# Kernel optimization log

Measured on AMD Instinct MI355X. Metric: run time of the kernel, lower is better.

Reference implementation:

```python
import jax, jax.numpy as jnp
import numpy as np

SCALE = 8.0  # sqrt(head_dim=64); module divides scores by self.scale


def setup_inputs() -> dict:
    key = jax.random.key(0)
    kq, kk, kv = jax.random.split(key, 3)
    B, H, L, D = 4, 8, 2048, 64
    queries = jax.random.normal(kq, (B, H, L, D), dtype=jnp.float32)
    keys = jax.random.normal(kk, (B, H, L, D), dtype=jnp.float32)
    values = jax.random.normal(kv, (B, H, L, D), dtype=jnp.float32)
    return {"queries": queries, "keys": keys, "values": values}


def reference(queries, keys, values):
    # scores: [B, H, L_Q, L_K]
    L_Q, L_K = queries.shape[2], keys.shape[2]
    scores = jnp.einsum('bnqd,bnkd->bnqk', queries, keys) / SCALE
    # causal mask: triu(ones, diagonal=1) positions set to -inf
    causal = jnp.triu(jnp.ones((L_Q, L_K), dtype=bool), k=1)
    scores = jnp.where(causal[None, None, :, :], -jnp.inf, scores)
    A = jax.nn.softmax(scores, axis=-1)  # dropout p=0.0 (eval) -> identity
    V = jnp.einsum('bnqk,bnkd->bnqd', A, values)
    return V
```

## Files before the change

kernel.cpp:

```cpp
#include <hip/hip_runtime.h>
#include <hip/hip_bf16.h>

typedef __attribute__((ext_vector_type(8))) short bf16x8;
typedef __attribute__((ext_vector_type(16))) float f32x16;

#define DHEAD 64
#define L_SEQ 2048
#define QSCALE (0.125f * 1.44269504088896340736f)

union U4S8 { uint4 u; bf16x8 s; };

__device__ __forceinline__ unsigned pk2(float a, float b) {
    unsigned r;
    asm("v_cvt_pk_bf16_f32 %0, %1, %2" : "=v"(r) : "v"(a), "v"(b));
    return r;
}

__device__ __forceinline__ float fexp2(float x) {
#if __has_builtin(__builtin_amdgcn_exp2f)
    return __builtin_amdgcn_exp2f(x);
#else
    return __expf(x * 0.69314718055994530942f);
#endif
}

#define MAX16(P) fmaxf(fmaxf(fmaxf(fmaxf(P[0],P[1]),fmaxf(P[2],P[3])),          \
                             fmaxf(fmaxf(P[4],P[5]),fmaxf(P[6],P[7]))),         \
                       fmaxf(fmaxf(fmaxf(P[8],P[9]),fmaxf(P[10],P[11])),        \
                             fmaxf(fmaxf(P[12],P[13]),fmaxf(P[14],P[15]))))
#define SUM16(P) ((((P[0]+P[1])+(P[2]+P[3]))+((P[4]+P[5])+(P[6]+P[7])))         \
                + (((P[8]+P[9])+(P[10]+P[11]))+((P[12]+P[13])+(P[14]+P[15]))))


__global__ __launch_bounds__(256, 2)
void fattn_kernel(const float* __restrict__ Qg, const float* __restrict__ Kg,
                  const float* __restrict__ Vg, float* __restrict__ Og) {
    __shared__ uint4 sK4[2][16][64];
    __shared__ uint4 sV4[2][16][64];

    const int tid  = threadIdx.x;
    const int lane = tid & 63;
    const int w    = tid >> 6;
    const int hi   = lane >> 5;
    const int c    = lane & 31;

    const int id  = blockIdx.x;
    const int bh  = (id & 7) + 8 * ((id >> 3) & 3);
    const int u_  = id >> 5;
    const int T   = (u_ < 8) ? (15 - u_) : (u_ - 8);

    const size_t base = (size_t)bh * L_SEQ * DHEAD;
    const int nt  = T + 1;
    const int q0w = T * 128 + w * 32;

    bf16x8 qf[4];
    {
        const float* Qrow = Qg + base + (size_t)(q0w + c) * DHEAD;
        #pragma unroll
        for (int kc = 0; kc < 4; ++kc) {
            float4 aa = *(const float4*)(Qrow + kc * 16 + hi * 8);
            float4 bb = *(const float4*)(Qrow + kc * 16 + hi * 8 + 4);
            U4S8 t;
            t.u = make_uint4(pk2(aa.x * QSCALE, aa.y * QSCALE),
                             pk2(aa.z * QSCALE, aa.w * QSCALE),
                             pk2(bb.x * QSCALE, bb.y * QSCALE),
                             pk2(bb.z * QSCALE, bb.w * QSCALE));
            qf[kc] = t.s;
        }
    }

    const float* Kpb = Kg + base + (size_t)(32 * w + c) * DHEAD + 32 * hi;
    const float* Vpb = Vg + base + (size_t)(32 * w + 16 * hi) * DHEAD + c;

    float4 rk[8];
    float  rv[32];

    auto load_tile = [&](int kt) {
        const float* Kp = Kpb + (size_t)kt * 128 * DHEAD;
        #pragma unroll
        for (int t = 0; t < 8; ++t) rk[t] = *(const float4*)(Kp + 4 * t);
        const float* Vp = Vpb + (size_t)kt * 128 * DHEAD;
        #pragma unroll
        for (int j = 0; j < 16; ++j) {
            rv[j]      = Vp[j * DHEAD];
            rv[16 + j] = Vp[j * DHEAD + 32];
        }
    };

    auto write_tile = [&](int nb) {
        #pragma unroll
        for (int q = 0; q < 2; ++q)
            #pragma unroll
            for (int hh = 0; hh < 2; ++hh) {
                const float4 r0 = rk[4 * q + 2 * hh], r1 = rk[4 * q + 2 * hh + 1];
                sK4[nb][w * 4 + 2 * hi + q][hh * 32 + c] =
                    make_uint4(pk2(r0.x, r0.y), pk2(r0.z, r0.w),
                               pk2(r1.x, r1.y), pk2(r1.z, r1.w));
            }
        #pragma unroll
        for (int dt = 0; dt < 2; ++dt)
            #pragma unroll
            for (int hh = 0; hh < 2; ++hh) {
                const int b = 16 * dt + 8 * hh;
                sV4[nb][(2 * w + hi) * 2 + dt][hh * 32 + c] =
                    make_uint4(pk2(rv[b + 0], rv[b + 1]), pk2(rv[b + 2], rv[b + 3]),
                               pk2(rv[b + 4], rv[b + 5]), pk2(rv[b + 6], rv[b + 7]));
            }
    };

    f32x16 o0 = {0,0,0,0,0,0,0,0,0,0,0,0,0,0,0,0};
    f32x16 o1 = o0;
    float m_r = -1e30f, l_r = 0.f;

    load_tile(0);
    write_tile(0);
    __syncthreads();

    for (int kt = 0; kt < nt; ++kt) {
        const int  cur = kt & 1;
        const bool pf  = (kt + 1 < nt);
        if (pf) load_tile(kt + 1);

        const bool diag = (kt == T);
        const int  nkb  = diag ? (w + 1) : 4;

        float p[4][16];

        __builtin_amdgcn_s_setprio(1);
        #pragma unroll
        for (int kb = 0; kb < 4; ++kb) {
            if (kb < nkb) {
                f32x16 s = {0,0,0,0,0,0,0,0,0,0,0,0,0,0,0,0};
                #pragma unroll
                for (int kc = 0; kc < 4; ++kc) {
                    U4S8 t; t.u = sK4[cur][kb * 4 + kc][lane];
                    s = __builtin_amdgcn_mfma_f32_32x32x16_bf16(t.s, qf[kc], s, 0, 0, 0);
                }
                #pragma unroll
                for (int r = 0; r < 16; ++r) p[kb][r] = s[r];
            }
        }
        __builtin_amdgcn_s_setprio(0);

        #pragma unroll
        for (int kb = 0; kb < 4; ++kb) {
            if (diag && kb == w) {
                #pragma unroll
                for (int r = 0; r < 16; ++r) {
                    const int kk = (r & 3) + 8 * (r >> 2) + 4 * hi;
                    if (kk > c) p[kb][r] = -1e30f;
                }
            }
        }

        float mx = MAX16(p[0]);
        if (nkb > 1) {
            float mxb = (nkb > 2) ? fmaxf(MAX16(p[1]),
                                          (nkb > 3) ? fmaxf(MAX16(p[2]), MAX16(p[3]))
                                                    : MAX16(p[2]))
                                  : MAX16(p[1]);
            mx = fmaxf(mx, mxb);
        }
        mx = fmaxf(mx, __shfl_xor(mx, 32));

        if (__any(mx > m_r + 8.f)) {
            const float mn    = fmaxf(m_r, mx);
            const float alpha = fexp2(m_r - mn);
            m_r  = mn;
            l_r *= alpha;
            #pragma unroll
            for (int r = 0; r < 16; ++r) {
                const float ab = __shfl(alpha, (r & 3) + 8 * (r >> 2) + 4 * hi);
                o0[r] *= ab; o1[r] *= ab;
            }
        }

        #pragma unroll
        for (int kb = 0; kb < 4; ++kb) {
            if (kb < nkb) {
                #pragma unroll
                for (int r = 0; r < 16; ++r) p[kb][r] = fexp2(p[kb][r] - m_r);
            }
        }
        float rs = SUM16(p[0]);
        if (nkb > 1) {
            float rsb = (nkb > 2) ? ((nkb > 3) ? (SUM16(p[1]) + (SUM16(p[2]) + SUM16(p[3])))
                                               : (SUM16(p[1]) + SUM16(p[2])))
                                  : SUM16(p[1]);
            rs += rsb;
        }
        rs += __shfl_xor(rs, 32);
        l_r += rs;

        __builtin_amdgcn_s_setprio(1);
        #pragma unroll
        for (int kc = 0; kc < 8; ++kc) {
            if (kc < 2 * nkb) {
                const int kb = kc >> 1, bs = (kc & 1) * 8;
                unsigned a0 = pk2(p[kb][bs + 0], p[kb][bs + 1]);
                unsigned a1 = pk2(p[kb][bs + 2], p[kb][bs + 3]);
                unsigned b0 = pk2(p[kb][bs + 4], p[kb][bs + 5]);
                unsigned b1 = pk2(p[kb][bs + 6], p[kb][bs + 7]);
                asm("v_permlane32_swap_b32 %0, %1" : "+v"(a0), "+v"(b0));
                asm("v_permlane32_swap_b32 %0, %1" : "+v"(a1), "+v"(b1));
                U4S8 t;
                t.u = make_uint4(a0, a1, b0, b1);
                U4S8 tv0; tv0.u = sV4[cur][kc * 2][lane];
                o0 = __builtin_amdgcn_mfma_f32_32x32x16_bf16(t.s, tv0.s, o0, 0, 0, 0);
                U4S8 tv1; tv1.u = sV4[cur][kc * 2 + 1][lane];
                o1 = __builtin_amdgcn_mfma_f32_32x32x16_bf16(t.s, tv1.s, o1, 0, 0, 0);
            }
        }
        __builtin_amdgcn_s_setprio(0);

        if (pf) write_tile(cur ^ 1);
        __syncthreads();
    }

    const float linv = 1.f / l_r;
    float* Op = Og + base;
    #pragma unroll
    for (int r = 0; r < 16; ++r) {
        const int   cr  = (r & 3) + 8 * (r >> 2) + 4 * hi;
        const float lb  = __shfl(linv, cr);
        const int   row = q0w + cr;
        Op[(size_t)row * DHEAD + c]      = o0[r] * lb;
        Op[(size_t)row * DHEAD + 32 + c] = o1[r] * lb;
    }
}

extern "C" void kernel_launch(void* const* d_in, const int* in_sizes, int n_in,
                              void* d_out, int out_size, void* d_ws, size_t ws_size,
                              hipStream_t stream) {
    const float* Q = (const float*)d_in[0];
    const float* K = (const float*)d_in[1];
    const float* V = (const float*)d_in[2];
    float* O = (float*)d_out;
    fattn_kernel<<<dim3(512), dim3(256), 0, stream>>>(Q, K, V, O);
}
```

Before: 52.72 us.

## Pair causal query tiles per block and split KV across two wave groups

Each block now processes two complementary query tiles (T and 15-T) in sequence, so every block does the same total causal work. Blocks grow to 512 threads, and the two 4-wave groups split alternate KV tiles. Their partial softmax states are merged through shared memory before each output store. This is meant to remove tail imbalance across blocks and halve the grid, at the cost of extra merge synchronisation, idle groups on odd tile counts, and more shared memory per block.

```diff
diff --git a/kernel.cpp b/kernel.cpp
--- a/kernel.cpp
+++ b/kernel.cpp
@@ -32,30 +32,30 @@
                 + (((P[8]+P[9])+(P[10]+P[11]))+((P[12]+P[13])+(P[14]+P[15]))))
 
 
-__global__ __launch_bounds__(256, 2)
+__global__ __launch_bounds__(512, 2)
 void fattn_kernel(const float* __restrict__ Qg, const float* __restrict__ Kg,
                   const float* __restrict__ Vg, float* __restrict__ Og) {
-    __shared__ uint4 sK4[2][16][64];
-    __shared__ uint4 sV4[2][16][64];
+    __shared__ uint4 sB[2][64][64];
 
     const int tid  = threadIdx.x;
     const int lane = tid & 63;
     const int w    = tid >> 6;
+    const int grp  = w >> 2;
+    const int wq   = w & 3;
     const int hi   = lane >> 5;
     const int c    = lane & 31;
 
     const int id  = blockIdx.x;
     const int bh  = (id & 7) + 8 * ((id >> 3) & 3);
-    const int u_  = id >> 5;
-    const int T   = (u_ < 8) ? (15 - u_) : (u_ - 8);
+    const int pr  = id >> 5;
+    const int T0  = pr, T1 = 15 - pr;
+    const int ph0 = (T0 + 2) >> 1;
 
     const size_t base = (size_t)bh * L_SEQ * DHEAD;
-    const int nt  = T + 1;
-    const int q0w = T * 128 + w * 32;
 
     bf16x8 qf[4];
-    {
-        const float* Qrow = Qg + base + (size_t)(q0w + c) * DHEAD;
+    auto loadQ = [&](int T) {
+        const float* Qrow = Qg + base + (size_t)(T * 128 + wq * 32 + c) * DHEAD;
         #pragma unroll
         for (int kc = 0; kc < 4; ++kc) {
             float4 aa = *(const float4*)(Qrow + kc * 16 + hi * 8);
@@ -67,7 +67,7 @@
                              pk2(bb.z * QSCALE, bb.w * QSCALE));
             qf[kc] = t.s;
         }
-    }
+    };
 
     const float* Kpb = Kg + base + (size_t)(32 * w + c) * DHEAD + 32 * hi;
     const float* Vpb = Vg + base + (size_t)(32 * w + 16 * hi) * DHEAD + c;
@@ -75,11 +75,11 @@
     float4 rk[8];
     float  rv[32];
 
-    auto load_tile = [&](int kt) {
-        const float* Kp = Kpb + (size_t)kt * 128 * DHEAD;
+    auto load_pair = [&](int jp) {
+        const float* Kp = Kpb + (size_t)jp * 256 * DHEAD;
         #pragma unroll
         for (int t = 0; t < 8; ++t) rk[t] = *(const float4*)(Kp + 4 * t);
-        const float* Vp = Vpb + (size_t)kt * 128 * DHEAD;
+        const float* Vp = Vpb + (size_t)jp * 256 * DHEAD;
         #pragma unroll
         for (int j = 0; j < 16; ++j) {
             rv[j]      = Vp[j * DHEAD];
@@ -87,13 +87,13 @@
         }
     };
 
-    auto write_tile = [&](int nb) {
+    auto write_pair = [&](int nb) {
         #pragma unroll
         for (int q = 0; q < 2; ++q)
             #pragma unroll
             for (int hh = 0; hh < 2; ++hh) {
                 const float4 r0 = rk[4 * q + 2 * hh], r1 = rk[4 * q + 2 * hh + 1];
-                sK4[nb][w * 4 + 2 * hi + q][hh * 32 + c] =
+                sB[nb][grp * 16 + wq * 4 + 2 * hi + q][hh * 32 + c] =
                     make_uint4(pk2(r0.x, r0.y), pk2(r0.z, r0.w),
                                pk2(r1.x, r1.y), pk2(r1.z, r1.w));
             }
@@ -102,7 +102,7 @@
             #pragma unroll
             for (int hh = 0; hh < 2; ++hh) {
                 const int b = 16 * dt + 8 * hh;
-                sV4[nb][(2 * w + hi) * 2 + dt][hh * 32 + c] =
+                sB[nb][32 + grp * 16 + (2 * wq + hi) * 2 + dt][hh * 32 + c] =
                     make_uint4(pk2(rv[b + 0], rv[b + 1]), pk2(rv[b + 2], rv[b + 3]),
                                pk2(rv[b + 4], rv[b + 5]), pk2(rv[b + 6], rv[b + 7]));
             }
@@ -112,121 +112,162 @@
     f32x16 o1 = o0;
     float m_r = -1e30f, l_r = 0.f;
 
-    load_tile(0);
-    write_tile(0);
+    auto merge_store_reset = [&](int T, int dead) {
+        float* scr = (float*)&sB[dead][0][0];
+        const int sidx = (wq * 64 + lane) * 35;
+        if (grp == 1) {
+            #pragma unroll
+            for (int r = 0; r < 16; ++r) {
+                scr[sidx + r]      = o0[r];
+                scr[sidx + 16 + r] = o1[r];
+            }
+            scr[sidx + 32] = m_r;
+            scr[sidx + 33] = l_r;
+        }
+        __syncthreads();
+        if (grp == 0) {
+            const float mO = scr[sidx + 32], lO = scr[sidx + 33];
+            const float mN = fmaxf(m_r, mO);
+            const float aE = fexp2(m_r - mN), aO = fexp2(mO - mN);
+            const float lN = aE * l_r + aO * lO;
+            const float linv = 1.f / lN;
+            float* Op = Og + base;
+            const int q0 = T * 128 + wq * 32;
+            #pragma unroll
+            for (int r = 0; r < 16; ++r) {
+                const int   cr = (r & 3) + 8 * (r >> 2) + 4 * hi;
+                const float bE = __shfl(aE, cr), bO = __shfl(aO, cr);
+                const float bl = __shfl(linv, cr);
+                const int   row = q0 + cr;
+                Op[(size_t)row * DHEAD + c]      = (bE * o0[r] + bO * scr[sidx + r]) * bl;
+                Op[(size_t)row * DHEAD + 32 + c] = (bE * o1[r] + bO * scr[sidx + 16 + r]) * bl;
+            }
+        }
+        __syncthreads();
+        #pragma unroll
+        for (int r = 0; r < 16; ++r) { o0[r] = 0.f; o1[r] = 0.f; }
+        m_r = -1e30f; l_r = 0.f;
+    };
+
+    loadQ(T0);
+    load_pair(0);
+    write_pair(0);
     __syncthreads();
-
-    for (int kt = 0; kt < nt; ++kt) {
-        const int  cur = kt & 1;
-        const bool pf  = (kt + 1 < nt);
-        if (pf) load_tile(kt + 1);
-
-        const bool diag = (kt == T);
-        const int  nkb  = diag ? (w + 1) : 4;
-
-        float p[4][16];
-
-        __builtin_amdgcn_s_setprio(1);
-        #pragma unroll
-        for (int kb = 0; kb < 4; ++kb) {
-            if (kb < nkb) {
-                f32x16 s = {0,0,0,0,0,0,0,0,0,0,0,0,0,0,0,0};
-                #pragma unroll
-                for (int kc = 0; kc < 4; ++kc) {
-                    U4S8 t; t.u = sK4[cur][kb * 4 + kc][lane];
-                    s = __builtin_amdgcn_mfma_f32_32x32x16_bf16(t.s, qf[kc], s, 0, 0, 0);
-                }
-                #pragma unroll
-                for (int r = 0; r < 16; ++r) p[kb][r] = s[r];
-            }
-        }
-        __builtin_amdgcn_s_setprio(0);
-
-        #pragma unroll
-        for (int kb = 0; kb < 4; ++kb) {
-            if (diag && kb == w) {
+    int buf = 0;
+
+    for (int ph = 0; ph < 9; ++ph) {
+        const bool inB = (ph >= ph0);
+        const int  T   = inB ? T1 : T0;
+        const int  jp  = inB ? ph - ph0 : ph;
+        const bool pf  = (ph + 1 < 9);
+        if (pf) load_pair((ph + 1 >= ph0) ? ph + 1 - ph0 : ph + 1);
+
+        if (ph == ph0) {
+            merge_store_reset(T0, buf ^ 1);
+            loadQ(T1);
+        }
+
+        const int kt = 2 * jp + grp;
+        if (kt <= T) {
+            const bool diag = (kt == T);
+            const int  nkb  = diag ? (wq + 1) : 4;
+
+            float p[4][16];
+
+            __builtin_amdgcn_s_setprio(1);
+            #pragma unroll
+            for (int kb = 0; kb < 4; ++kb) {
+                if (kb < nkb) {
+                    f32x16 s = {0,0,0,0,0,0,0,0,0,0,0,0,0,0,0,0};
+                    #pragma unroll
+                    for (int kc = 0; kc < 4; ++kc) {
+                        U4S8 t; t.u = sB[buf][grp * 16 + kb * 4 + kc][lane];
+                        s = __builtin_amdgcn_mfma_f32_32x32x16_bf16(t.s, qf[kc], s, 0, 0, 0);
+                    }
+                    #pragma unroll
+                    for (int r = 0; r < 16; ++r) p[kb][r] = s[r];
+                }
+            }
+            __builtin_amdgcn_s_setprio(0);
+
+            #pragma unroll
+            for (int kb = 0; kb < 4; ++kb) {
+                if (diag && kb == wq) {
+                    #pragma unroll
+                    for (int r = 0; r < 16; ++r) {
+                        const int kk = (r & 3) + 8 * (r >> 2) + 4 * hi;
+                        if (kk > c) p[kb][r] = -1e30f;
+                    }
+                }
+            }
+
+            float mx = MAX16(p[0]);
+            if (nkb > 1) {
+                float mxb = (nkb > 2) ? fmaxf(MAX16(p[1]),
+                                              (nkb > 3) ? fmaxf(MAX16(p[2]), MAX16(p[3]))
+                                                        : MAX16(p[2]))
+                                      : MAX16(p[1]);
+                mx = fmaxf(mx, mxb);
+            }
+            mx = fmaxf(mx, __shfl_xor(mx, 32));
+
+            if (__any(mx > m_r + 8.f)) {
+                const float mn    = fmaxf(m_r, mx);
+                const float alpha = fexp2(m_r - mn);
+                m_r  = mn;
+                l_r *= alpha;
                 #pragma unroll
                 for (int r = 0; r < 16; ++r) {
-                    const int kk = (r & 3) + 8 * (r >> 2) + 4 * hi;
-                    if (kk > c) p[kb][r] = -1e30f;
-                }
-            }
-        }
-
-        float mx = MAX16(p[0]);
-        if (nkb > 1) {
-            float mxb = (nkb > 2) ? fmaxf(MAX16(p[1]),
-                                          (nkb > 3) ? fmaxf(MAX16(p[2]), MAX16(p[3]))
-                                                    : MAX16(p[2]))
-                                  : MAX16(p[1]);
-            mx = fmaxf(mx, mxb);
-        }
-        mx = fmaxf(mx, __shfl_xor(mx, 32));
-
-        if (__any(mx > m_r + 8.f)) {
-            const float mn    = fmaxf(m_r, mx);
-            const float alpha = fexp2(m_r - mn);
-            m_r  = mn;
-            l_r *= alpha;
-            #pragma unroll
-            for (int r = 0; r < 16; ++r) {
-                const float ab = __shfl(alpha, (r & 3) + 8 * (r >> 2) + 4 * hi);
-                o0[r] *= ab; o1[r] *= ab;
-            }
-        }
-
-        #pragma unroll
-        for (int kb = 0; kb < 4; ++kb) {
-            if (kb < nkb) {
-                #pragma unroll
-                for (int r = 0; r < 16; ++r) p[kb][r] = fexp2(p[kb][r] - m_r);
-            }
-        }
-        float rs = SUM16(p[0]);
-        if (nkb > 1) {
-            float rsb = (nkb > 2) ? ((nkb > 3) ? (SUM16(p[1]) + (SUM16(p[2]) + SUM16(p[3])))
-                                               : (SUM16(p[1]) + SUM16(p[2])))
-                                  : SUM16(p[1]);
-            rs += rsb;
-        }
-        rs += __shfl_xor(rs, 32);
-        l_r += rs;
-
-        __builtin_amdgcn_s_setprio(1);
-        #pragma unroll
-        for (int kc = 0; kc < 8; ++kc) {
-            if (kc < 2 * nkb) {
-                const int kb = kc >> 1, bs = (kc & 1) * 8;
-                unsigned a0 = pk2(p[kb][bs + 0], p[kb][bs + 1]);
-                unsigned a1 = pk2(p[kb][bs + 2], p[kb][bs + 3]);
-                unsigned b0 = pk2(p[kb][bs + 4], p[kb][bs + 5]);
-                unsigned b1 = pk2(p[kb][bs + 6], p[kb][bs + 7]);
-                asm("v_permlane32_swap_b32 %0, %1" : "+v"(a0), "+v"(b0));
-                asm("v_permlane32_swap_b32 %0, %1" : "+v"(a1), "+v"(b1));
-                U4S8 t;
-                t.u = make_uint4(a0, a1, b0, b1);
-                U4S8 tv0; tv0.u = sV4[cur][kc * 2][lane];
-                o0 = __builtin_amdgcn_mfma_f32_32x32x16_bf16(t.s, tv0.s, o0, 0, 0, 0);
-                U4S8 tv1; tv1.u = sV4[cur][kc * 2 + 1][lane];
-                o1 = __builtin_amdgcn_mfma_f32_32x32x16_bf16(t.s, tv1.s, o1, 0, 0, 0);
-            }
-        }
-        __builtin_amdgcn_s_setprio(0);
-
-        if (pf) write_tile(cur ^ 1);
+                    const float ab = __shfl(alpha, (r & 3) + 8 * (r >> 2) + 4 * hi);
+                    o0[r] *= ab; o1[r] *= ab;
+                }
+            }
+
+            #pragma unroll
+            for (int kb = 0; kb < 4; ++kb) {
+                if (kb < nkb) {
+                    #pragma unroll
+                    for (int r = 0; r < 16; ++r) p[kb][r] = fexp2(p[kb][r] - m_r);
+                }
+            }
+            float rs = SUM16(p[0]);
+            if (nkb > 1) {
+                float rsb = (nkb > 2) ? ((nkb > 3) ? (SUM16(p[1]) + (SUM16(p[2]) + SUM16(p[3])))
+                                                   : (SUM16(p[1]) + SUM16(p[2])))
+                                      : SUM16(p[1]);
+                rs += rsb;
+            }
+            rs += __shfl_xor(rs, 32);
+            l_r += rs;
+
+            __builtin_amdgcn_s_setprio(1);
+            #pragma unroll
+            for (int kc = 0; kc < 8; ++kc) {
+                if (kc < 2 * nkb) {
+                    const int kb = kc >> 1, bs = (kc & 1) * 8;
+                    unsigned a0 = pk2(p[kb][bs + 0], p[kb][bs + 1]);
+                    unsigned a1 = pk2(p[kb][bs + 2], p[kb][bs + 3]);
+                    unsigned b0 = pk2(p[kb][bs + 4], p[kb][bs + 5]);
+                    unsigned b1 = pk2(p[kb][bs + 6], p[kb][bs + 7]);
+                    asm("v_permlane32_swap_b32 %0, %1" : "+v"(a0), "+v"(b0));
+                    asm("v_permlane32_swap_b32 %0, %1" : "+v"(a1), "+v"(b1));
+                    U4S8 t;
+                    t.u = make_uint4(a0, a1, b0, b1);
+                    U4S8 tv0; tv0.u = sB[buf][32 + grp * 16 + kc * 2][lane];
+                    o0 = __builtin_amdgcn_mfma_f32_32x32x16_bf16(t.s, tv0.s, o0, 0, 0, 0);
+                    U4S8 tv1; tv1.u = sB[buf][32 + grp * 16 + kc * 2 + 1][lane];
+                    o1 = __builtin_amdgcn_mfma_f32_32x32x16_bf16(t.s, tv1.s, o1, 0, 0, 0);
+                }
+            }
+            __builtin_amdgcn_s_setprio(0);
+        }
+
+        if (pf) write_pair(buf ^ 1);
         __syncthreads();
+        buf ^= 1;
     }
 
-    const float linv = 1.f / l_r;
-    float* Op = Og + base;
-    #pragma unroll
-    for (int r = 0; r < 16; ++r) {
-        const int   cr  = (r & 3) + 8 * (r >> 2) + 4 * hi;
-        const float lb  = __shfl(linv, cr);
-        const int   row = q0w + cr;
-        Op[(size_t)row * DHEAD + c]      = o0[r] * lb;
-        Op[(size_t)row * DHEAD + 32 + c] = o1[r] * lb;
-    }
+    merge_store_reset(T1, buf);
 }
 
 extern "C" void kernel_launch(void* const* d_in, const int* in_sizes, int n_in,
@@ -236,5 +277,5 @@
     const float* K = (const float*)d_in[1];
     const float* V = (const float*)d_in[2];
     float* O = (float*)d_out;
-    fattn_kernel<<<dim3(512), dim3(256), 0, stream>>>(Q, K, V, O);
-}
+    fattn_kernel<<<dim3(256), dim3(512), 0, stream>>>(Q, K, V, O);
+}
```

After: 55.59 us. +5.4%, slower.
